# Kernel tuning notes

Measured on AMD Instinct MI355X. Metric: run time of the kernel, lower is better.

Reference implementation:

```python
import jax, jax.numpy as jnp
import numpy as np

MUL = 64            # multiplicity of 0e and 1o in node_feats
NUM_RADIAL = 8      # number of 0e edge scalars (MLP input)
AVG_NEIGH = 16.0
INV_SQRT3 = float(1.0 / np.sqrt(3.0))  # w3j(1,1,0) contraction coefficient

# e3nn.normalize_function constant for silu: c = 1/sqrt(E_{z~N(0,1)}[silu(z)^2])
_gh_x, _gh_w = np.polynomial.hermite_e.hermegauss(128)
_gh_w = _gh_w / _gh_w.sum()
_silu_np = _gh_x / (1.0 + np.exp(-_gh_x))
ACT_CST = float(1.0 / np.sqrt(np.sum(_gh_w * _silu_np ** 2)))


def _mlp(x, ws):
    # path gradient normalization: x <- (1/sqrt(fan_in)) * x @ W, W ~ N(0,1)
    for i, w in enumerate(ws):
        x = (x @ w) * (1.0 / np.sqrt(w.shape[0]))
        if i < len(ws) - 1:
            x = jax.nn.silu(x) * ACT_CST  # normalized activation
    return x


def setup_inputs() -> dict:
    key = jax.random.key(0)
    ks = jax.random.split(key, 8)
    n_nodes, n_edges = 20000, 320000
    node_dim = MUL + MUL * 3          # 64x0e + 64x1o -> 256
    edge_dim = NUM_RADIAL + 3         # 8x0e + 1x1o   -> 11
    return {
        "node_feats": jax.random.normal(ks[0], (n_nodes, node_dim), jnp.float32),
        "edge_attrs": jax.random.normal(ks[1], (n_edges, edge_dim), jnp.float32),
        "senders": jax.random.randint(ks[2], (n_edges,), 0, n_nodes),
        "receivers": jax.random.randint(ks[3], (n_edges,), 0, n_nodes),
        # MLP weights: [8->64, 64->64, 64->64, 64->256] (256 = num_irreps of messages)
        "w0": jax.random.normal(ks[4], (NUM_RADIAL, 64), jnp.float32),
        "w1": jax.random.normal(ks[5], (64, 64), jnp.float32),
        "w2": jax.random.normal(ks[6], (64, 64), jnp.float32),
        "w3": jax.random.normal(ks[7], (64, 2 * MUL + 2 * MUL), jnp.float32),
    }


def reference(node_feats, edge_attrs, senders, receivers, w0, w1, w2, w3):
    N = node_feats.shape[0]
    # split node features into 64x0e scalars and 64x1o vectors
    s = node_feats[:, :MUL]                        # [N, 64]
    v = node_feats[:, MUL:].reshape(N, MUL, 3)     # [N, 64, 3]
    # gather by sender
    ms = s[senders]                                # [E, 64]
    mv = v[senders]                                # [E, 64, 3]
    # split edge attrs: 8x0e scalars (MLP input), 1x1o sh vector (TP input)
    es = edge_attrs[:, :NUM_RADIAL]                # [E, 8]
    ev = edge_attrs[:, NUM_RADIAL:]                # [E, 3]
    # equivariant tensor product, filtered to target irreps {0e, 1o}:
    #   0e (x) 1o -> 1o : coefficient 1 (sqrt(3) * w3j(0,1,1))
    tp_v = ms[:, :, None] * ev[:, None, :]         # [E, 64, 3]
    #   1o (x) 1o -> 0e : dot / sqrt(3)
    tp_s = jnp.einsum("emc,ec->em", mv, ev) * INV_SQRT3  # [E, 64]
    # concatenate + regroup -> 128x0e + 128x1o
    msg_s = jnp.concatenate([ms, tp_s], axis=-1)   # [E, 128]
    msg_v = jnp.concatenate([mv, tp_v], axis=1)    # [E, 128, 3]
    # MLP gate: one scalar per irrep (256 total), broadcast over m components
    mix = _mlp(es, (w0, w1, w2, w3))               # [E, 256]
    msg_s = msg_s * mix[:, : 2 * MUL]
    msg_v = msg_v * mix[:, 2 * MUL :][:, :, None]
    # scatter-add into receivers
    out_s = jax.ops.segment_sum(msg_s, receivers, num_segments=N)  # [N, 128]
    out_v = jax.ops.segment_sum(msg_v, receivers, num_segments=N)  # [N, 128, 3]
    out = jnp.concatenate([out_s, out_v.reshape(N, -1)], axis=-1)  # [N, 512]
    return out * (1.0 / np.sqrt(AVG_NEIGH))
```

## Files before the change

kernel.cpp:

```cpp
#include <hip/hip_runtime.h>

typedef __attribute__((ext_vector_type(8))) __bf16 bf16x8;
typedef __attribute__((ext_vector_type(8))) _Float16 half8;
typedef __attribute__((ext_vector_type(4))) float f32x4;

#define HP 72
#define MIXP 264
#define MAXDEG 64

__device__ __forceinline__ float silu_n(float x) {
    return x / (1.0f + __expf(-x)) * 1.6765444f;
}

__device__ __forceinline__ unsigned short f2b(float f) {
    unsigned int u = __float_as_uint(f);
    u += 0x7FFF + ((u >> 16) & 1);
    return (unsigned short)(u >> 16);
}
__device__ __forceinline__ float b2f(unsigned short u) {
    return __uint_as_float(((unsigned int)u) << 16);
}


__global__ __launch_bounds__(256) void init_prep(
    int* __restrict__ wptr, int N,
    const float* __restrict__ w0, const float* __restrict__ w1,
    const float* __restrict__ w2, const float* __restrict__ w3,
    _Float16* __restrict__ w0t,
    __bf16* __restrict__ w1t, __bf16* __restrict__ w2t, __bf16* __restrict__ w3t)
{
    const int tid0 = blockIdx.x * 256 + threadIdx.x;
    const int stride = gridDim.x * 256;
    for (int n = tid0; n < N; n += stride) wptr[n] = n * MAXDEG;
    for (int id = tid0; id < 2048; id += stride) {
        int j = id & 7, f = id >> 3;
        int lane = f & 63, c = f >> 6;
        int n = c * 16 + (lane & 15);
        int k = (lane >> 4) * 8 + j;
        w0t[id] = (k < 8) ? (_Float16)(w0[k * 64 + n] * 0.35355339f) : (_Float16)0.f;
    }
    for (int id = tid0; id < 4096; id += stride) {
        int j = id & 7, f = id >> 3;
        int lane = f & 63, g = f >> 6;
        int c = g >> 1, s = g & 1;
        int n = c * 16 + (lane & 15);
        int k = s * 32 + (lane >> 4) * 8 + j;
        w1t[id] = (__bf16)(w1[k * 64 + n] * 0.125f);
        w2t[id] = (__bf16)(w2[k * 64 + n] * 0.125f);
    }
    for (int id = tid0; id < 16384; id += stride) {
        int j = id & 7, f = id >> 3;
        int lane = f & 63, g = f >> 6;
        int wch = g >> 3, c = (g >> 1) & 3, s = g & 1;
        int n = wch * 64 + c * 16 + (lane & 15);
        int k = s * 32 + (lane >> 4) * 8 + j;
        w3t[id] = (__bf16)(w3[k * 256 + n] * 0.03125f);
    }
}


__global__ void scatter_pad(const int* __restrict__ rcv, int* __restrict__ wptr,
                            int* __restrict__ perm, int E) {
    int e = blockIdx.x * blockDim.x + threadIdx.x;
    if (e < E) {
        int r = rcv[e];
        int p = atomicAdd(&wptr[r], 1);
        if (p < r * MAXDEG + MAXDEG) perm[p] = e;
    }
}


__global__ __launch_bounds__(256, 4) void mlp_mfma(
    const float* __restrict__ ea,
    float4*      __restrict__ evq,
    unsigned short* __restrict__ mixb,
    const _Float16* __restrict__ w0t,
    const __bf16* __restrict__ w1t,
    const __bf16* __restrict__ w2t,
    const __bf16* __restrict__ w3t,
    int E)
{
    __shared__ char smem[64 * HP * 2 * 2];
    __shared__ float eas[64 * 12];
    __bf16* hA = (__bf16*)smem;
    __bf16* hB = hA + 64 * HP;
    unsigned short* mixs = (unsigned short*)smem;

    const int t = threadIdx.x;
    const int lane = t & 63;
    const int wv = t >> 6;
    const int quad = lane >> 4;
    const int l15 = lane & 15;
    const int pbase = blockIdx.x * 64;
    const int nval = min(E - pbase, 64);

    for (int idx = t; idx < 704; idx += 256) {
        int sl = idx / 11;
        int f = idx - sl * 11;
        eas[sl * 12 + f] = (sl < nval) ? ea[(size_t)(pbase + sl) * 11 + f] : 0.f;
    }
    __syncthreads();
    if (t < nval)
        evq[pbase + t] = make_float4(eas[t * 12 + 8], eas[t * 12 + 9],
                                     eas[t * 12 + 10], 0.f);

    {
        const int m0 = wv * 16;
        half8 A0;
        #pragma unroll
        for (int j = 0; j < 8; j++) A0[j] = (_Float16)0.f;
        if (quad == 0) {
            const float* er = &eas[(m0 + l15) * 12];
            #pragma unroll
            for (int j = 0; j < 8; j++) A0[j] = (_Float16)er[j];
        }
        #pragma unroll
        for (int c = 0; c < 4; c++) {
            half8 B0 = *(const half8*)(w0t + (size_t)(c * 64 + lane) * 8);
            f32x4 a = {0.f, 0.f, 0.f, 0.f};
            a = __builtin_amdgcn_mfma_f32_16x16x32_f16(A0, B0, a, 0, 0, 0);
            #pragma unroll
            for (int r = 0; r < 4; r++)
                hA[(m0 + quad * 4 + r) * HP + c * 16 + l15] = (__bf16)silu_n(a[r]);
        }
    }

    auto layer = [&](const __bf16* src, __bf16* dst, const __bf16* wt) {
        const int m0 = wv * 16;
        const __bf16* arow = src + (m0 + l15) * HP;
        bf16x8 A0 = *(const bf16x8*)(arow + quad * 8);
        bf16x8 A1 = *(const bf16x8*)(arow + 32 + quad * 8);
        #pragma unroll
        for (int c = 0; c < 4; c++) {
            bf16x8 B0 = *(const bf16x8*)(wt + ((c * 2 + 0) * 64 + lane) * 8);
            bf16x8 B1 = *(const bf16x8*)(wt + ((c * 2 + 1) * 64 + lane) * 8);
            f32x4 a = {0.f, 0.f, 0.f, 0.f};
            a = __builtin_amdgcn_mfma_f32_16x16x32_bf16(A0, B0, a, 0, 0, 0);
            a = __builtin_amdgcn_mfma_f32_16x16x32_bf16(A1, B1, a, 0, 0, 0);
            #pragma unroll
            for (int r = 0; r < 4; r++) {
                dst[(m0 + quad * 4 + r) * HP + c * 16 + l15] = (__bf16)silu_n(a[r]);
            }
        }
    };

    layer(hA, hB, w1t);
    layer(hB, hA, w2t);

    __syncthreads();

    f32x4 acc[4][4];
    {
        bf16x8 B[4][2];
        #pragma unroll
        for (int c = 0; c < 4; c++)
            #pragma unroll
            for (int s = 0; s < 2; s++)
                B[c][s] = *(const bf16x8*)(w3t + ((((wv * 4 + c) * 2) + s) * 64 + lane) * 8);

        #pragma unroll
        for (int m = 0; m < 4; m++)
            #pragma unroll
            for (int c = 0; c < 4; c++)
                acc[m][c] = (f32x4){0.f, 0.f, 0.f, 0.f};

        #pragma unroll
        for (int m = 0; m < 4; m++) {
            const __bf16* arow = hA + (m * 16 + l15) * HP;
            bf16x8 A0 = *(const bf16x8*)(arow + quad * 8);
            bf16x8 A1 = *(const bf16x8*)(arow + 32 + quad * 8);
            #pragma unroll
            for (int c = 0; c < 4; c++) {
                acc[m][c] = __builtin_amdgcn_mfma_f32_16x16x32_bf16(A0, B[c][0], acc[m][c], 0, 0, 0);
                acc[m][c] = __builtin_amdgcn_mfma_f32_16x16x32_bf16(A1, B[c][1], acc[m][c], 0, 0, 0);
            }
        }
    }

    #pragma unroll
    for (int half = 0; half < 2; half++) {
        __syncthreads();
        #pragma unroll
        for (int mm = 0; mm < 2; mm++) {
            int m = half * 2 + mm;
            #pragma unroll
            for (int c = 0; c < 4; c++)
                #pragma unroll
                for (int r = 0; r < 4; r++)
                    mixs[(mm * 16 + quad * 4 + r) * MIXP + wv * 64 + c * 16 + l15] =
                        f2b(acc[m][c][r]);
        }
        __syncthreads();
        #pragma unroll
        for (int rr = 0; rr < 8; rr++) {
            int row = wv * 8 + rr;
            int grow = pbase + half * 32 + row;
            if (grow < E) {
                ushort4 v;
                v.x = mixs[row * MIXP + lane];
                v.y = mixs[row * MIXP + 64 + lane];
                v.z = mixs[row * MIXP + 128 + lane];
                v.w = mixs[row * MIXP + 192 + lane];
                *(ushort4*)(mixb + (size_t)grow * 256 + lane * 4) = v;
            }
        }
    }
}


__global__ __launch_bounds__(256) void gather_1wave(
    const float* __restrict__ nf,
    const int*   __restrict__ snd,
    const int*   __restrict__ wptr,
    const int*   __restrict__ perm,
    const float4* __restrict__ evq,
    const unsigned short* __restrict__ mixb,
    float* __restrict__ out, int N)
{
    const int t = threadIdx.x;
    const int lane = t & 63;
    const int wv = t >> 6;
    const int n = blockIdx.x * 4 + wv;
    if (n >= N) return;
    const int p0 = n * MAXDEG;
    const int deg = min(wptr[n] - p0, MAXDEG);

    int eL = 0, sL = 0;
    float4 evL = make_float4(0.f, 0.f, 0.f, 0.f);
    if (lane < deg) {
        eL = perm[p0 + lane];
        sL = snd[eL];
        evL = evq[eL];
    }

    float s1 = 0.f, s2 = 0.f;
    float a10 = 0.f, a11 = 0.f, a12 = 0.f;
    float a20 = 0.f, a21 = 0.f, a22 = 0.f;

    for (int i = 0; i < deg; i++) {
        const int e = __shfl(eL, i);
        const int s = __shfl(sL, i);
        const float evx = __shfl(evL.x, i);
        const float evy = __shfl(evL.y, i);
        const float evz = __shfl(evL.z, i);
        ushort4 mm = *(const ushort4*)(mixb + (size_t)e * 256 + lane * 4);
        float m0 = b2f(mm.x);
        float m1 = b2f(mm.y);
        float m2 = b2f(mm.z);
        float m3 = b2f(mm.w);
        const float* nrow = nf + (size_t)s * 256;
        float sv = nrow[lane];
        const float* vr = nrow + 64 + 3 * lane;
        float v0 = vr[0], v1 = vr[1], v2 = vr[2];

        s1 += sv * m0;
        s2 += (v0 * evx + v1 * evy + v2 * evz) * m1;
        a10 += v0 * m2; a11 += v1 * m2; a12 += v2 * m2;
        float tt = sv * m3;
        a20 += tt * evx; a21 += tt * evy; a22 += tt * evz;
    }

    float* orow = out + (size_t)n * 512;
    orow[lane] = s1;
    orow[64 + lane] = s2 * 0.57735027f;
    float* o1 = orow + 128 + 3 * lane;
    o1[0] = a10; o1[1] = a11; o1[2] = a12;
    float* o2 = orow + 320 + 3 * lane;
    o2[0] = a20; o2[1] = a21; o2[2] = a22;
}


#define BLOCK 128
__device__ __forceinline__ void atomAddF(float* p, float v) { unsafeAtomicAdd(p, v); }

__global__ void __launch_bounds__(BLOCK) fused_mp(
    const float* __restrict__ nf, const float* __restrict__ ea,
    const int* __restrict__ snd, const int* __restrict__ rcv,
    const float* __restrict__ w0, const float* __restrict__ w1,
    const float* __restrict__ w2, const float* __restrict__ w3,
    float* __restrict__ out, int E)
{
    __shared__ float lds_h[BLOCK * 64];
    __shared__ float lds_st[BLOCK * 64];
    const int tid = threadIdx.x;
    const int lane = tid & 63;
    const int wv = tid >> 6;
    const int ebase = blockIdx.x * BLOCK;
    const int e = ebase + tid;
    const bool valid = e < E;

    float es[8];
    float ev0 = 0.f, ev1 = 0.f, ev2 = 0.f;
    int sidx = 0, ridx = 0;
    if (valid) {
        const float* p = ea + (size_t)e * 11;
        #pragma unroll
        for (int k = 0; k < 8; k++) es[k] = p[k];
        ev0 = p[8]; ev1 = p[9]; ev2 = p[10];
        sidx = snd[e]; ridx = rcv[e];
    } else {
        #pragma unroll
        for (int k = 0; k < 8; k++) es[k] = 0.f;
    }
    for (int j = 0; j < 64; j++) {
        float a = 0.f;
        #pragma unroll
        for (int k = 0; k < 8; k++) a += es[k] * w0[k * 64 + j];
        lds_h[j * BLOCK + tid] = silu_n(a * 0.35355339f);
    }
    float acc[64];
    #pragma unroll
    for (int j = 0; j < 64; j++) acc[j] = 0.f;
    for (int k = 0; k < 64; k++) {
        float hk = lds_h[k * BLOCK + tid];
        const float* wr = w1 + k * 64;
        #pragma unroll
        for (int j = 0; j < 64; j++) acc[j] += hk * wr[j];
    }
    #pragma unroll
    for (int j = 0; j < 64; j++) lds_h[j * BLOCK + tid] = silu_n(acc[j] * 0.125f);
    #pragma unroll
    for (int j = 0; j < 64; j++) acc[j] = 0.f;
    for (int k = 0; k < 64; k++) {
        float hk = lds_h[k * BLOCK + tid];
        const float* wr = w2 + k * 64;
        #pragma unroll
        for (int j = 0; j < 64; j++) acc[j] += hk * wr[j];
    }
    #pragma unroll
    for (int j = 0; j < 64; j++) lds_h[j * BLOCK + tid] = silu_n(acc[j] * 0.125f);

    const int wave_base = ebase + wv * 64;
    int wn = E - wave_base;
    const int wave_nvalid = wn < 0 ? 0 : (wn > 64 ? 64 : wn);
    float* st = lds_st + wv * 64 * 64;

    auto compute_chunk = [&](int c) {
        #pragma unroll
        for (int j = 0; j < 64; j++) acc[j] = 0.f;
        for (int k = 0; k < 64; k++) {
            float hk = lds_h[k * BLOCK + tid];
            const float* wr = w3 + k * 256 + c * 64;
            #pragma unroll
            for (int j = 0; j < 64; j++) acc[j] += hk * wr[j];
        }
        #pragma unroll
        for (int j = 0; j < 64; j++) st[j * 64 + (lane ^ j)] = acc[j] * (0.125f * 0.25f);
    };

    compute_chunk(0);
    for (int i = 0; i < wave_nvalid; i++) {
        int sI = __shfl(sidx, i);
        int rI = __shfl(ridx, i);
        float m = st[lane * 64 + (i ^ lane)];
        atomAddF(&out[(size_t)rI * 512 + lane], nf[(size_t)sI * 256 + lane] * m);
    }
    compute_chunk(1);
    for (int i = 0; i < wave_nvalid; i++) {
        int sI = __shfl(sidx, i);
        int rI = __shfl(ridx, i);
        float a0 = __shfl(ev0, i), a1 = __shfl(ev1, i), a2 = __shfl(ev2, i);
        const float* vr = nf + (size_t)sI * 256 + 64 + 3 * lane;
        float d = vr[0] * a0 + vr[1] * a1 + vr[2] * a2;
        float m = st[lane * 64 + (i ^ lane)];
        atomAddF(&out[(size_t)rI * 512 + 64 + lane], d * 0.57735027f * m);
    }
    compute_chunk(2);
    for (int i = 0; i < wave_nvalid; i++) {
        int sI = __shfl(sidx, i);
        int rI = __shfl(ridx, i);
        const float* vr = nf + (size_t)sI * 256 + 64 + 3 * lane;
        float m = st[lane * 64 + (i ^ lane)];
        float* orow = out + (size_t)rI * 512 + 128 + 3 * lane;
        atomAddF(orow + 0, vr[0] * m);
        atomAddF(orow + 1, vr[1] * m);
        atomAddF(orow + 2, vr[2] * m);
    }
    compute_chunk(3);
    for (int i = 0; i < wave_nvalid; i++) {
        int sI = __shfl(sidx, i);
        int rI = __shfl(ridx, i);
        float a0 = __shfl(ev0, i), a1 = __shfl(ev1, i), a2 = __shfl(ev2, i);
        float sv = nf[(size_t)sI * 256 + lane];
        float m = st[lane * 64 + (i ^ lane)];
        float* orow = out + (size_t)rI * 512 + 320 + 3 * lane;
        atomAddF(orow + 0, sv * a0 * m);
        atomAddF(orow + 1, sv * a1 * m);
        atomAddF(orow + 2, sv * a2 * m);
    }
}


static inline size_t al256(size_t x) { return (x + 255) & ~(size_t)255; }

extern "C" void kernel_launch(void* const* d_in, const int* in_sizes, int n_in,
                              void* d_out, int out_size, void* d_ws, size_t ws_size,
                              hipStream_t stream)
{
    const float* nf = (const float*)d_in[0];
    const float* ea = (const float*)d_in[1];
    const int*   sn = (const int*)  d_in[2];
    const int*   rc = (const int*)  d_in[3];
    const float* w0 = (const float*)d_in[4];
    const float* w1 = (const float*)d_in[5];
    const float* w2 = (const float*)d_in[6];
    const float* w3 = (const float*)d_in[7];
    float* out = (float*)d_out;
    const int E = in_sizes[2];
    const int N = in_sizes[0] / 256;

    size_t o_wptr = 0;
    size_t o_perm = o_wptr + al256((size_t)(N + 1) * 4);
    size_t o_evq  = o_perm + al256((size_t)N * MAXDEG * 4);
    size_t o_mix  = o_evq  + al256((size_t)E * 16);
    size_t o_w1t  = o_mix  + al256((size_t)E * 512);
    size_t o_w2t  = o_w1t  + al256(4096 * 2);
    size_t o_w3t  = o_w2t  + al256(4096 * 2);
    size_t o_w0t  = o_w3t  + al256(16384 * 2);
    size_t need   = o_w0t  + 2048 * 2;

    if (ws_size < need) {
        hipMemsetAsync(d_out, 0, (size_t)out_size * sizeof(float), stream);
        const int blocks = (E + BLOCK - 1) / BLOCK;
        fused_mp<<<blocks, BLOCK, 0, stream>>>(nf, ea, sn, rc, w0, w1, w2, w3, out, E);
        return;
    }

    char* ws = (char*)d_ws;
    int* wptr = (int*)(ws + o_wptr);
    int* perm = (int*)(ws + o_perm);
    float4* evq = (float4*)(ws + o_evq);
    unsigned short* mixb = (unsigned short*)(ws + o_mix);
    __bf16* w1t = (__bf16*)(ws + o_w1t);
    __bf16* w2t = (__bf16*)(ws + o_w2t);
    __bf16* w3t = (__bf16*)(ws + o_w3t);
    _Float16* w0t = (_Float16*)(ws + o_w0t);

    init_prep<<<128, 256, 0, stream>>>(wptr, N, w0, w1, w2, w3, w0t, w1t, w2t, w3t);
    scatter_pad<<<(E + 255) / 256, 256, 0, stream>>>(rc, wptr, perm, E);
    mlp_mfma<<<(E + 63) / 64, 256, 0, stream>>>(
        ea, evq, mixb, w0t, w1t, w2t, w3t, E);
    gather_1wave<<<(N + 3) / 4, 256, 0, stream>>>(
        nf, sn, wptr, perm, evq, mixb, out, N);
}
```

Before: 251.2 us.

## Fuse edge MLP into per-node gather kernel, dropping mix buffer round-trip

Merges the edge MLP kernel and the receiver-side gather into one kernel where each wave handles one node and computes the MLP for its incoming edges in chunks of 16, keeping gate values in per-wave LDS. This removes the global write and re-read of the bf16 mix buffer (E×512 bytes) and the evq buffer, plus one kernel launch. In exchange, MFMA tiles are only partly filled when a chunk holds fewer than 16 edges, edge attributes are gathered randomly, weights are reloaded per pass, and the MLP now sits serially in each wave's path before its gather, reducing overlap.

Result: slower. 568.9 us (+126.5%).

```diff
diff --git a/kernel.cpp b/kernel.cpp
--- a/kernel.cpp
+++ b/kernel.cpp
@@ -7,6 +7,7 @@
 #define HP 72
 #define MIXP 264
 #define MAXDEG 64
+#define WREG 8448
 
 __device__ __forceinline__ float silu_n(float x) {
     return x / (1.0f + __expf(-x)) * 1.6765444f;
@@ -70,194 +71,155 @@
 }
 
 
-__global__ __launch_bounds__(256, 4) void mlp_mfma(
+__global__ __launch_bounds__(256) void fused_node(
+    const float* __restrict__ nf,
     const float* __restrict__ ea,
-    float4*      __restrict__ evq,
-    unsigned short* __restrict__ mixb,
+    const int*   __restrict__ snd,
+    const int*   __restrict__ wptr,
+    const int*   __restrict__ perm,
     const _Float16* __restrict__ w0t,
     const __bf16* __restrict__ w1t,
     const __bf16* __restrict__ w2t,
     const __bf16* __restrict__ w3t,
-    int E)
+    float* __restrict__ out, int N)
 {
-    __shared__ char smem[64 * HP * 2 * 2];
-    __shared__ float eas[64 * 12];
-    __bf16* hA = (__bf16*)smem;
-    __bf16* hB = hA + 64 * HP;
-    unsigned short* mixs = (unsigned short*)smem;
+    __shared__ char smem[4 * WREG];
+    __shared__ float eas[4][16 * 12];
+    __shared__ int eidxs[4][16];
 
     const int t = threadIdx.x;
     const int lane = t & 63;
     const int wv = t >> 6;
     const int quad = lane >> 4;
     const int l15 = lane & 15;
-    const int pbase = blockIdx.x * 64;
-    const int nval = min(E - pbase, 64);
-
-    for (int idx = t; idx < 704; idx += 256) {
-        int sl = idx / 11;
-        int f = idx - sl * 11;
-        eas[sl * 12 + f] = (sl < nval) ? ea[(size_t)(pbase + sl) * 11 + f] : 0.f;
-    }
-    __syncthreads();
-    if (t < nval)
-        evq[pbase + t] = make_float4(eas[t * 12 + 8], eas[t * 12 + 9],
-                                     eas[t * 12 + 10], 0.f);
-
-    {
-        const int m0 = wv * 16;
-        half8 A0;
-        #pragma unroll
-        for (int j = 0; j < 8; j++) A0[j] = (_Float16)0.f;
-        if (quad == 0) {
-            const float* er = &eas[(m0 + l15) * 12];
+    const int n = blockIdx.x * 4 + wv;
+    if (n >= N) return;
+
+    char* wbase = smem + wv * WREG;
+    __bf16* hA = (__bf16*)wbase;
+    __bf16* hB = (__bf16*)(wbase + 2304);
+    unsigned short* mixw = (unsigned short*)wbase;
+    float* easw = eas[wv];
+    int* eidw = eidxs[wv];
+
+    const int p0 = n * MAXDEG;
+    const int deg = min(wptr[n] - p0, MAXDEG);
+    const int npass = (deg + 15) >> 4;
+
+    float s1 = 0.f, s2 = 0.f;
+    float a10 = 0.f, a11 = 0.f, a12 = 0.f;
+    float a20 = 0.f, a21 = 0.f, a22 = 0.f;
+
+    for (int pass = 0; pass < npass; pass++) {
+        const int cnt = min(deg - pass * 16, 16);
+
+        int eL = 0, sL = 0;
+        if (lane < cnt) {
+            eL = perm[p0 + pass * 16 + lane];
+            sL = snd[eL];
+        }
+        if (lane < 16) eidw[lane] = eL;
+
+        for (int idx = lane; idx < 192; idx += 64) easw[idx] = 0.f;
+        for (int idx = lane; idx < cnt * 11; idx += 64) {
+            int i = idx / 11, f = idx - i * 11;
+            easw[i * 12 + f] = ea[(size_t)eidw[i] * 11 + f];
+        }
+
+        {
+            half8 A0;
             #pragma unroll
-            for (int j = 0; j < 8; j++) A0[j] = (_Float16)er[j];
-        }
-        #pragma unroll
-        for (int c = 0; c < 4; c++) {
-            half8 B0 = *(const half8*)(w0t + (size_t)(c * 64 + lane) * 8);
-            f32x4 a = {0.f, 0.f, 0.f, 0.f};
-            a = __builtin_amdgcn_mfma_f32_16x16x32_f16(A0, B0, a, 0, 0, 0);
+            for (int j = 0; j < 8; j++) A0[j] = (_Float16)0.f;
+            if (quad == 0) {
+                const float* er = &easw[l15 * 12];
+                #pragma unroll
+                for (int j = 0; j < 8; j++) A0[j] = (_Float16)er[j];
+            }
             #pragma unroll
-            for (int r = 0; r < 4; r++)
-                hA[(m0 + quad * 4 + r) * HP + c * 16 + l15] = (__bf16)silu_n(a[r]);
-        }
-    }
-
-    auto layer = [&](const __bf16* src, __bf16* dst, const __bf16* wt) {
-        const int m0 = wv * 16;
-        const __bf16* arow = src + (m0 + l15) * HP;
-        bf16x8 A0 = *(const bf16x8*)(arow + quad * 8);
-        bf16x8 A1 = *(const bf16x8*)(arow + 32 + quad * 8);
-        #pragma unroll
-        for (int c = 0; c < 4; c++) {
-            bf16x8 B0 = *(const bf16x8*)(wt + ((c * 2 + 0) * 64 + lane) * 8);
-            bf16x8 B1 = *(const bf16x8*)(wt + ((c * 2 + 1) * 64 + lane) * 8);
-            f32x4 a = {0.f, 0.f, 0.f, 0.f};
-            a = __builtin_amdgcn_mfma_f32_16x16x32_bf16(A0, B0, a, 0, 0, 0);
-            a = __builtin_amdgcn_mfma_f32_16x16x32_bf16(A1, B1, a, 0, 0, 0);
-            #pragma unroll
-            for (int r = 0; r < 4; r++) {
-                dst[(m0 + quad * 4 + r) * HP + c * 16 + l15] = (__bf16)silu_n(a[r]);
+            for (int c = 0; c < 4; c++) {
+                half8 B0 = *(const half8*)(w0t + (size_t)(c * 64 + lane) * 8);
+                f32x4 a = {0.f, 0.f, 0.f, 0.f};
+                a = __builtin_amdgcn_mfma_f32_16x16x32_f16(A0, B0, a, 0, 0, 0);
+                #pragma unroll
+                for (int r = 0; r < 4; r++)
+                    hA[(quad * 4 + r) * HP + c * 16 + l15] = (__bf16)silu_n(a[r]);
             }
         }
-    };
-
-    layer(hA, hB, w1t);
-    layer(hB, hA, w2t);
-
-    __syncthreads();
-
-    f32x4 acc[4][4];
-    {
-        bf16x8 B[4][2];
-        #pragma unroll
-        for (int c = 0; c < 4; c++)
-            #pragma unroll
-            for (int s = 0; s < 2; s++)
-                B[c][s] = *(const bf16x8*)(w3t + ((((wv * 4 + c) * 2) + s) * 64 + lane) * 8);
-
-        #pragma unroll
-        for (int m = 0; m < 4; m++)
-            #pragma unroll
-            for (int c = 0; c < 4; c++)
-                acc[m][c] = (f32x4){0.f, 0.f, 0.f, 0.f};
-
-        #pragma unroll
-        for (int m = 0; m < 4; m++) {
-            const __bf16* arow = hA + (m * 16 + l15) * HP;
+
+        auto layer = [&](const __bf16* src, __bf16* dst, const __bf16* wt) {
+            const __bf16* arow = src + l15 * HP;
             bf16x8 A0 = *(const bf16x8*)(arow + quad * 8);
             bf16x8 A1 = *(const bf16x8*)(arow + 32 + quad * 8);
             #pragma unroll
             for (int c = 0; c < 4; c++) {
-                acc[m][c] = __builtin_amdgcn_mfma_f32_16x16x32_bf16(A0, B[c][0], acc[m][c], 0, 0, 0);
-                acc[m][c] = __builtin_amdgcn_mfma_f32_16x16x32_bf16(A1, B[c][1], acc[m][c], 0, 0, 0);
+                bf16x8 B0 = *(const bf16x8*)(wt + ((c * 2 + 0) * 64 + lane) * 8);
+                bf16x8 B1 = *(const bf16x8*)(wt + ((c * 2 + 1) * 64 + lane) * 8);
+                f32x4 a = {0.f, 0.f, 0.f, 0.f};
+                a = __builtin_amdgcn_mfma_f32_16x16x32_bf16(A0, B0, a, 0, 0, 0);
+                a = __builtin_amdgcn_mfma_f32_16x16x32_bf16(A1, B1, a, 0, 0, 0);
+                #pragma unroll
+                for (int r = 0; r < 4; r++)
+                    dst[(quad * 4 + r) * HP + c * 16 + l15] = (__bf16)silu_n(a[r]);
             }
-        }
-    }
-
-    #pragma unroll
-    for (int half = 0; half < 2; half++) {
-        __syncthreads();
-        #pragma unroll
-        for (int mm = 0; mm < 2; mm++) {
-            int m = half * 2 + mm;
+        };
+        layer(hA, hB, w1t);
+        layer(hB, hA, w2t);
+
+        {
+            const __bf16* arow = hA + l15 * HP;
+            bf16x8 A0 = *(const bf16x8*)(arow + quad * 8);
+            bf16x8 A1 = *(const bf16x8*)(arow + 32 + quad * 8);
             #pragma unroll
-            for (int c = 0; c < 4; c++)
-                #pragma unroll
-                for (int r = 0; r < 4; r++)
-                    mixs[(mm * 16 + quad * 4 + r) * MIXP + wv * 64 + c * 16 + l15] =
-                        f2b(acc[m][c][r]);
-        }
-        __syncthreads();
-        #pragma unroll
-        for (int rr = 0; rr < 8; rr++) {
-            int row = wv * 8 + rr;
-            int grow = pbase + half * 32 + row;
-            if (grow < E) {
-                ushort4 v;
-                v.x = mixs[row * MIXP + lane];
-                v.y = mixs[row * MIXP + 64 + lane];
-                v.z = mixs[row * MIXP + 128 + lane];
-                v.w = mixs[row * MIXP + 192 + lane];
-                *(ushort4*)(mixb + (size_t)grow * 256 + lane * 4) = v;
+            for (int half = 0; half < 2; half++) {
+                f32x4 acc[2][4];
+                #pragma unroll
+                for (int wc = 0; wc < 2; wc++)
+                    #pragma unroll
+                    for (int c = 0; c < 4; c++)
+                        acc[wc][c] = (f32x4){0.f, 0.f, 0.f, 0.f};
+                #pragma unroll
+                for (int wc = 0; wc < 2; wc++) {
+                    const int wch = half * 2 + wc;
+                    #pragma unroll
+                    for (int c = 0; c < 4; c++) {
+                        bf16x8 B0 = *(const bf16x8*)(w3t + ((((wch * 4 + c) * 2) + 0) * 64 + lane) * 8);
+                        bf16x8 B1 = *(const bf16x8*)(w3t + ((((wch * 4 + c) * 2) + 1) * 64 + lane) * 8);
+                        acc[wc][c] = __builtin_amdgcn_mfma_f32_16x16x32_bf16(A0, B0, acc[wc][c], 0, 0, 0);
+                        acc[wc][c] = __builtin_amdgcn_mfma_f32_16x16x32_bf16(A1, B1, acc[wc][c], 0, 0, 0);
+                    }
+                }
+                #pragma unroll
+                for (int wc = 0; wc < 2; wc++)
+                    #pragma unroll
+                    for (int c = 0; c < 4; c++)
+                        #pragma unroll
+                        for (int r = 0; r < 4; r++)
+                            mixw[(quad * 4 + r) * MIXP + (half * 2 + wc) * 64 + c * 16 + l15] =
+                                f2b(acc[wc][c][r]);
             }
         }
-    }
-}
-
-
-__global__ __launch_bounds__(256) void gather_1wave(
-    const float* __restrict__ nf,
-    const int*   __restrict__ snd,
-    const int*   __restrict__ wptr,
-    const int*   __restrict__ perm,
-    const float4* __restrict__ evq,
-    const unsigned short* __restrict__ mixb,
-    float* __restrict__ out, int N)
-{
-    const int t = threadIdx.x;
-    const int lane = t & 63;
-    const int wv = t >> 6;
-    const int n = blockIdx.x * 4 + wv;
-    if (n >= N) return;
-    const int p0 = n * MAXDEG;
-    const int deg = min(wptr[n] - p0, MAXDEG);
-
-    int eL = 0, sL = 0;
-    float4 evL = make_float4(0.f, 0.f, 0.f, 0.f);
-    if (lane < deg) {
-        eL = perm[p0 + lane];
-        sL = snd[eL];
-        evL = evq[eL];
-    }
-
-    float s1 = 0.f, s2 = 0.f;
-    float a10 = 0.f, a11 = 0.f, a12 = 0.f;
-    float a20 = 0.f, a21 = 0.f, a22 = 0.f;
-
-    for (int i = 0; i < deg; i++) {
-        const int e = __shfl(eL, i);
-        const int s = __shfl(sL, i);
-        const float evx = __shfl(evL.x, i);
-        const float evy = __shfl(evL.y, i);
-        const float evz = __shfl(evL.z, i);
-        ushort4 mm = *(const ushort4*)(mixb + (size_t)e * 256 + lane * 4);
-        float m0 = b2f(mm.x);
-        float m1 = b2f(mm.y);
-        float m2 = b2f(mm.z);
-        float m3 = b2f(mm.w);
-        const float* nrow = nf + (size_t)s * 256;
-        float sv = nrow[lane];
-        const float* vr = nrow + 64 + 3 * lane;
-        float v0 = vr[0], v1 = vr[1], v2 = vr[2];
-
-        s1 += sv * m0;
-        s2 += (v0 * evx + v1 * evy + v2 * evz) * m1;
-        a10 += v0 * m2; a11 += v1 * m2; a12 += v2 * m2;
-        float tt = sv * m3;
-        a20 += tt * evx; a21 += tt * evy; a22 += tt * evz;
+
+        for (int i = 0; i < cnt; i++) {
+            const int s = __shfl(sL, i);
+            const float evx = easw[i * 12 + 8];
+            const float evy = easw[i * 12 + 9];
+            const float evz = easw[i * 12 + 10];
+            const unsigned short* mrow = mixw + i * MIXP;
+            float m0 = b2f(mrow[lane]);
+            float m1 = b2f(mrow[64 + lane]);
+            float m2 = b2f(mrow[128 + lane]);
+            float m3 = b2f(mrow[192 + lane]);
+            const float* nrow = nf + (size_t)s * 256;
+            float sv = nrow[lane];
+            const float* vr = nrow + 64 + 3 * lane;
+            float v0 = vr[0], v1 = vr[1], v2 = vr[2];
+
+            s1 += sv * m0;
+            s2 += (v0 * evx + v1 * evy + v2 * evz) * m1;
+            a10 += v0 * m2; a11 += v1 * m2; a12 += v2 * m2;
+            float tt = sv * m3;
+            a20 += tt * evx; a21 += tt * evy; a22 += tt * evz;
+        }
     }
 
     float* orow = out + (size_t)n * 512;
@@ -411,9 +373,7 @@
 
     size_t o_wptr = 0;
     size_t o_perm = o_wptr + al256((size_t)(N + 1) * 4);
-    size_t o_evq  = o_perm + al256((size_t)N * MAXDEG * 4);
-    size_t o_mix  = o_evq  + al256((size_t)E * 16);
-    size_t o_w1t  = o_mix  + al256((size_t)E * 512);
+    size_t o_w1t  = o_perm + al256((size_t)N * MAXDEG * 4);
     size_t o_w2t  = o_w1t  + al256(4096 * 2);
     size_t o_w3t  = o_w2t  + al256(4096 * 2);
     size_t o_w0t  = o_w3t  + al256(16384 * 2);
@@ -429,8 +389,6 @@
     char* ws = (char*)d_ws;
     int* wptr = (int*)(ws + o_wptr);
     int* perm = (int*)(ws + o_perm);
-    float4* evq = (float4*)(ws + o_evq);
-    unsigned short* mixb = (unsigned short*)(ws + o_mix);
     __bf16* w1t = (__bf16*)(ws + o_w1t);
     __bf16* w2t = (__bf16*)(ws + o_w2t);
     __bf16* w3t = (__bf16*)(ws + o_w3t);
@@ -438,8 +396,6 @@
 
     init_prep<<<128, 256, 0, stream>>>(wptr, N, w0, w1, w2, w3, w0t, w1t, w2t, w3t);
     scatter_pad<<<(E + 255) / 256, 256, 0, stream>>>(rc, wptr, perm, E);
-    mlp_mfma<<<(E + 63) / 64, 256, 0, stream>>>(
-        ea, evq, mixb, w0t, w1t, w2t, w3t, E);
-    gather_1wave<<<(N + 3) / 4, 256, 0, stream>>>(
-        nf, sn, wptr, perm, evq, mixb, out, N);
-}
+    fused_node<<<(N + 3) / 4, 256, 0, stream>>>(
+        nf, ea, sn, wptr, perm, w0t, w1t, w2t, w3t, out, N);
+}
```
